# Optimization experiments

Measured on AMD Instinct MI355X. Metric: run time of the kernel, lower is better.

## Reference

```python
import jax, jax.numpy as jnp
import numpy as np

B, S, H, NH = 2, 2048, 2048, 16
DH = H // NH


def setup_inputs() -> dict:
    key = jax.random.key(0)
    ks = jax.random.split(key, 9)
    scale = 1.0 / np.sqrt(H)
    inp = {
        "hidden_state": jax.random.normal(ks[0], (B, S, H), dtype=jnp.float32),
        "Wq": jax.random.normal(ks[1], (H, H), dtype=jnp.float32) * scale,
        "bq": jnp.zeros((H,), dtype=jnp.float32),
        "Wk": jax.random.normal(ks[2], (H, H), dtype=jnp.float32) * scale,
        "bk": jnp.zeros((H,), dtype=jnp.float32),
        "Wv": jax.random.normal(ks[3], (H, H), dtype=jnp.float32) * scale,
        "bv": jnp.zeros((H,), dtype=jnp.float32),
        "Wo": jax.random.normal(ks[4], (H, H), dtype=jnp.float32) * scale,
        "bo": jnp.zeros((H,), dtype=jnp.float32),
    }
    # additive causal mask: 0 on/below diagonal, large negative above
    neg = jnp.float32(-1e9)
    tri = jnp.tril(jnp.ones((S, S), dtype=bool))
    inp["causal_mask"] = jnp.where(tri, 0.0, neg)[None, None, :, :]
    return inp


def reference(hidden_state, Wq, bq, Wk, bk, Wv, bv, Wo, bo, causal_mask):
    def split_heads(x):  # [B,S,H] -> [B,NH,S,DH]
        return x.reshape(B, S, NH, DH).transpose(0, 2, 1, 3)

    q = split_heads(hidden_state @ Wq + bq)
    k = split_heads(hidden_state @ Wk + bk)
    v = split_heads(hidden_state @ Wv + bv)

    scores = jnp.einsum("bhqd,bhkd->bhqk", q, k) / jnp.sqrt(jnp.float32(DH))
    scores = scores + causal_mask
    probs = jax.nn.softmax(scores, axis=-1)
    out = jnp.einsum("bhqk,bhkd->bhqd", probs, v)  # [B,NH,S,DH]
    out = out.transpose(0, 2, 1, 3).reshape(B, S, H)
    return out @ Wo + bo
```

## Files before the change

kernel.cpp:

```cpp
#include <hip/hip_runtime.h>
#include <cstdint>

typedef __attribute__((ext_vector_type(4))) float f32x4;
typedef __attribute__((ext_vector_type(16))) float f32x16;
typedef __attribute__((ext_vector_type(8))) __bf16 bf16x8;
typedef __attribute__((ext_vector_type(4))) unsigned short u16x4;
typedef __attribute__((ext_vector_type(2))) unsigned int u32x2;
typedef __attribute__((ext_vector_type(4))) float fvec4;

#define DEV __device__ __forceinline__
#define MFMA16(a, b, c) __builtin_amdgcn_mfma_f32_16x16x32_bf16((a), (b), (c), 0, 0, 0)
#define MFMA32(a, b, c) __builtin_amdgcn_mfma_f32_32x32x16_bf16((a), (b), (c), 0, 0, 0)

DEV unsigned short f2bf(float f) {
  union { float f; uint32_t u; } c; c.f = f;
  uint32_t u = c.u;
  return (unsigned short)((u + 0x7FFFu + ((u >> 16) & 1u)) >> 16);
}

DEV unsigned int pack2(float lo, float hi) {
  union { float f; uint32_t u; } a, b;
  a.f = lo; b.f = hi;
  return __builtin_amdgcn_perm(b.u + 0x8000u, a.u + 0x8000u, 0x07060302u);
}

DEV void gll16(const void* g, void* l) {
  __builtin_amdgcn_global_load_lds(
      (const __attribute__((address_space(1))) void*)(uintptr_t)g,
      (__attribute__((address_space(3))) void*)(uint32_t)(uintptr_t)l,
      16, 0, 0);
}

__global__ void cvt_bf16(const float* __restrict__ src, unsigned short* __restrict__ dst) {
  int i = (blockIdx.x * 256 + threadIdx.x) * 4;
  fvec4 v = *(const fvec4*)(src + i);
  u16x4 o;
  o[0] = f2bf(v[0]); o[1] = f2bf(v[1]); o[2] = f2bf(v[2]); o[3] = f2bf(v[3]);
  *(u16x4*)(dst + i) = o;
}

__global__ void transpose_cvt4(const float* __restrict__ W0, const float* __restrict__ W1,
                               const float* __restrict__ W2, const float* __restrict__ W3,
                               unsigned short* __restrict__ Dqkv, unsigned short* __restrict__ Do) {
  __shared__ float t[32][33];
  const float* W = blockIdx.z == 0 ? W0 : blockIdx.z == 1 ? W1 : blockIdx.z == 2 ? W2 : W3;
  unsigned short* WT = blockIdx.z < 3 ? Dqkv + (size_t)blockIdx.z * 2048 * 2048 : Do;
  int n0 = blockIdx.x * 32, k0 = blockIdx.y * 32;
  int x = threadIdx.x, y = threadIdx.y;
  #pragma unroll
  for (int i = 0; i < 32; i += 8)
    t[y + i][x] = W[(size_t)(k0 + y + i) * 2048 + n0 + x];
  __syncthreads();
  #pragma unroll
  for (int i = 0; i < 32; i += 8)
    WT[(size_t)(n0 + y + i) * 2048 + k0 + x] = f2bf(t[x][y + i]);
}

constexpr float QSC = 0.08838834764831845f * 1.4426950408889634f;

template <int MODE>
__global__ __launch_bounds__(256, 2) void gemm128(
    const unsigned short* __restrict__ A,
    const unsigned short* __restrict__ Bt,
    const float* __restrict__ b0, const float* __restrict__ b1,
    const float* __restrict__ b2,
    void* __restrict__ o0, void* __restrict__ o1, void* __restrict__ o2) {
  __shared__ unsigned short As[128 * 64];
  __shared__ unsigned short Bs[128 * 64];
  const int id = blockIdx.x;
  const int m0 = (((id & 7) << 2) | ((id >> 3) & 3)) * 128;
  const int n0 = (id >> 5) * 128;
  const int tid = threadIdx.x;
  const int wave = tid >> 6, lid = tid & 63;
  const int l16 = lid & 15, lq = lid >> 4;
  const int wm = (wave >> 1) * 64, wn = (wave & 1) * 64;

  const int srow = lid >> 3;
  const int sgrp = (lid & 7) ^ srow;

  f32x4 acc[4][4] = {};

  for (int k0 = 0; k0 < 2048; k0 += 64) {
    #pragma unroll
    for (int i = 0; i < 4; ++i) {
      const int t = wave * 4 + i;
      const int r = t * 8 + srow;
      gll16(A + (size_t)(m0 + r) * 2048 + k0 + sgrp * 8, (char*)As + t * 1024 + lid * 16);
      gll16(Bt + (size_t)(n0 + r) * 2048 + k0 + sgrp * 8, (char*)Bs + t * 1024 + lid * 16);
    }
    __syncthreads();
    #pragma unroll
    for (int kk = 0; kk < 2; ++kk) {
      const int G = kk * 4 + lq;
      bf16x8 af[4], bfr[4];
      #pragma unroll
      for (int i = 0; i < 4; ++i)
        af[i] = *(const bf16x8*)(As + (wm + i * 16 + l16) * 64 + ((G ^ (l16 & 7)) << 3));
      #pragma unroll
      for (int j = 0; j < 4; ++j)
        bfr[j] = *(const bf16x8*)(Bs + (wn + j * 16 + l16) * 64 + ((G ^ (l16 & 7)) << 3));
      #pragma unroll
      for (int i = 0; i < 4; ++i)
        #pragma unroll
        for (int j = 0; j < 4; ++j)
          acc[i][j] = MFMA16(af[i], bfr[j], acc[i][j]);
    }
    __syncthreads();
  }

  #pragma unroll
  for (int j = 0; j < 4; ++j) {
    const int c = n0 + wn + j * 16 + l16;
    if (MODE == 1) {
      const int which = c >> 11;
      const int hd = c & 2047;
      const int h = hd >> 7, d = hd & 127;
      const float* bp = which == 0 ? b0 : which == 1 ? b1 : b2;
      const float bv = bp[hd];
      if (which == 2) {
        #pragma unroll
        for (int i = 0; i < 4; ++i) {
          const int row0 = m0 + wm + i * 16 + lq * 4;
          const int bb = row0 >> 11, s0 = row0 & 2047;
          u16x4 pv;
          #pragma unroll
          for (int r = 0; r < 4; ++r) pv[r] = f2bf(acc[i][j][r] + bv);
          *(u16x4*)((unsigned short*)o2 + ((size_t)((bb * 16 + h) * 128 + d)) * 2048 + s0) = pv;
        }
      } else {
        const float sc = which == 0 ? QSC : 1.0f;
        unsigned short* op = which == 0 ? (unsigned short*)o0 : (unsigned short*)o1;
        #pragma unroll
        for (int i = 0; i < 4; ++i) {
          #pragma unroll
          for (int r = 0; r < 4; ++r) {
            const int row = m0 + wm + i * 16 + lq * 4 + r;
            const int bb = row >> 11, s = row & 2047;
            op[(size_t)((bb * 16 + h) * 2048 + s) * 128 + d] = f2bf((acc[i][j][r] + bv) * sc);
          }
        }
      }
    } else {
      const float bv = b0[c];
      #pragma unroll
      for (int i = 0; i < 4; ++i)
        #pragma unroll
        for (int r = 0; r < 4; ++r) {
          const int row = m0 + wm + i * 16 + lq * 4 + r;
          ((float*)o0)[(size_t)row * 2048 + c] = acc[i][j][r] + bv;
        }
    }
  }
}

__global__ __launch_bounds__(256, 2) void attn(
    const unsigned short* __restrict__ Q,
    const unsigned short* __restrict__ K,
    const unsigned short* __restrict__ Vt,
    unsigned short* __restrict__ ctx) {
  __shared__ unsigned short Ks[64 * 128];
  __shared__ unsigned short Vts[128 * 64];
  __shared__ unsigned short Ps[4 * 32 * 64];

  const int bh = blockIdx.y;
  const int jq = (bh < 16) ? (15 - (int)blockIdx.x) : (int)blockIdx.x;
  const int q0 = jq * 128;
  const int b = bh >> 4, h = bh & 15;
  const unsigned short* Qh = Q + (size_t)bh * 2048 * 128;
  const unsigned short* Kh = K + (size_t)bh * 2048 * 128;
  const unsigned short* Vth = Vt + (size_t)bh * 128 * 2048;

  const int tid = threadIdx.x;
  const int wave = tid >> 6, lid = tid & 63;
  const int l32 = lid & 31, half = lid >> 5;
  const int qrow = q0 + wave * 32 + l32;
  unsigned short* Pw = Ps + wave * 2048 + l32 * 64;
  const int qsw = l32 & 7;

  bf16x8 qf[8];
  #pragma unroll
  for (int ds = 0; ds < 8; ++ds)
    qf[ds] = *(const bf16x8*)(Qh + (size_t)qrow * 128 + ds * 16 + half * 8);

  float m_i = -1e30f, l_i = 0.f;
  f32x16 acc[4] = {};

  const int ntiles = 2 * jq + 2;
  for (int jt = 0; jt < ntiles; ++jt) {
    const int k0 = jt * 64;
    #pragma unroll
    for (int ii = 0; ii < 4; ++ii) {
      const int t = wave * 4 + ii;
      const int r = t * 4 + (lid >> 4);
      const int g = (lid & 15) ^ (r & 15);
      gll16(Kh + (size_t)(k0 + r) * 128 + g * 8, (char*)Ks + t * 1024 + lid * 16);
    }
    #pragma unroll
    for (int ii = 0; ii < 4; ++ii) {
      const int t = wave * 4 + ii;
      const int d = t * 8 + (lid >> 3);
      const int g = (lid & 7) ^ (d & 7);
      gll16(Vth + (size_t)d * 2048 + k0 + g * 8, (char*)Vts + t * 1024 + lid * 16);
    }
    __syncthreads();

    f32x16 sacc[2] = {};
    #pragma unroll
    for (int ds = 0; ds < 8; ++ds) {
      #pragma unroll
      for (int mb = 0; mb < 2; ++mb) {
        const int kr = mb * 32 + l32;
        bf16x8 af = *(const bf16x8*)(Ks + kr * 128 + (((ds * 2 + half) ^ (kr & 15)) << 3));
        sacc[mb] = MFMA32(af, qf[ds], sacc[mb]);
      }
    }

    if (jt >= 2 * jq) {
      #pragma unroll
      for (int mb = 0; mb < 2; ++mb)
        #pragma unroll
        for (int i = 0; i < 16; ++i) {
          const int kg = k0 + mb * 32 + (i & 3) + 8 * (i >> 2) + 4 * half;
          if (kg > qrow) sacc[mb][i] = -1e30f;
        }
    }

    float tmax = -1e30f;
    #pragma unroll
    for (int mb = 0; mb < 2; ++mb)
      #pragma unroll
      for (int i = 0; i < 16; ++i) tmax = fmaxf(tmax, sacc[mb][i]);
    tmax = fmaxf(tmax, __shfl_xor(tmax, 32));

    const float mnew = fmaxf(m_i, tmax);
    const float alpha = exp2f(m_i - mnew);
    m_i = mnew;

    float ps = 0.f;
    #pragma unroll
    for (int mb = 0; mb < 2; ++mb) {
      #pragma unroll
      for (int i = 0; i < 16; ++i) {
        sacc[mb][i] = exp2f(sacc[mb][i] - mnew);
        ps += sacc[mb][i];
      }
      #pragma unroll
      for (int u = 0; u < 4; ++u) {
        u32x2 w;
        w[0] = pack2(sacc[mb][4 * u], sacc[mb][4 * u + 1]);
        w[1] = pack2(sacc[mb][4 * u + 2], sacc[mb][4 * u + 3]);
        *(u32x2*)(Pw + (((u + mb * 4) ^ qsw) << 3) + half * 4) = w;
      }
    }
    ps += __shfl_xor(ps, 32);
    l_i = l_i * alpha + ps;
    #pragma unroll
    for (int db = 0; db < 4; ++db)
      #pragma unroll
      for (int i = 0; i < 16; ++i) acc[db][i] *= alpha;

    #pragma unroll
    for (int ks = 0; ks < 4; ++ks) {
      bf16x8 pf = *(const bf16x8*)(Pw + (((ks * 2 + half) ^ qsw) << 3));
      #pragma unroll
      for (int db = 0; db < 4; ++db) {
        const int d = db * 32 + l32;
        bf16x8 vf = *(const bf16x8*)(Vts + d * 64 + (((ks * 2 + half) ^ (d & 7)) << 3));
        acc[db] = MFMA32(vf, pf, acc[db]);
      }
    }
    __syncthreads();
  }

  const float inv = 1.f / l_i;
  const size_t base = ((size_t)(b * 2048 + qrow)) * 2048 + h * 128;
  #pragma unroll
  for (int db = 0; db < 4; ++db) {
    #pragma unroll
    for (int u = 0; u < 4; ++u) {
      u32x2 w;
      w[0] = pack2(acc[db][4 * u] * inv, acc[db][4 * u + 1] * inv);
      w[1] = pack2(acc[db][4 * u + 2] * inv, acc[db][4 * u + 3] * inv);
      *(u32x2*)(ctx + base + db * 32 + 8 * u + 4 * half) = w;
    }
  }
}

extern "C" void kernel_launch(void* const* d_in, const int* in_sizes, int n_in,
                              void* d_out, int out_size, void* d_ws, size_t ws_size,
                              hipStream_t stream) {
  const float* hs = (const float*)d_in[0];
  const float* Wq = (const float*)d_in[1];
  const float* bq = (const float*)d_in[2];
  const float* Wk = (const float*)d_in[3];
  const float* bk = (const float*)d_in[4];
  const float* Wv = (const float*)d_in[5];
  const float* bv = (const float*)d_in[6];
  const float* Wo = (const float*)d_in[7];
  const float* bo = (const float*)d_in[8];
  float* out = (float*)d_out;

  char* ws = (char*)d_ws;
  unsigned short* hsb   = (unsigned short*)(ws);
  unsigned short* wqkvt = (unsigned short*)(ws + (16 << 20));
  unsigned short* wot   = (unsigned short*)(ws + (40 << 20));
  unsigned short* Qb    = (unsigned short*)(ws + (48 << 20));
  unsigned short* Kb    = (unsigned short*)(ws + (64 << 20));
  unsigned short* Vtb   = (unsigned short*)(ws + (80 << 20));
  unsigned short* ctx   = (unsigned short*)(ws + (96 << 20));

  cvt_bf16<<<dim3(8192), dim3(256), 0, stream>>>(hs, hsb);
  transpose_cvt4<<<dim3(64, 64, 4), dim3(32, 8), 0, stream>>>(Wq, Wk, Wv, Wo, wqkvt, wot);

  gemm128<1><<<dim3(1536), 256, 0, stream>>>(hsb, wqkvt, bq, bk, bv,
                                             (void*)Qb, (void*)Kb, (void*)Vtb);
  attn<<<dim3(16, 32), 256, 0, stream>>>(Qb, Kb, Vtb, ctx);
  gemm128<0><<<dim3(512), 256, 0, stream>>>(ctx, wot, bo, nullptr, nullptr,
                                            (void*)out, nullptr, nullptr);
}
```

Baseline: 380.1 us.

## Halve attention query tile, pass P via lane shuffles, fuse prologue kernels

The attention kernel now uses 64-query blocks with 2 waves (128 threads) and a 32x32 grid, which doubles the block count for better load balance across the causal triangle. The new head-pair ordering also changes the work ordering. The probability tile no longer goes through LDS: P fragments are exchanged between wave halves with __shfl_xor, which removes the Ps buffer and its LDS traffic. The hidden-state conversion and the weight transposes are merged into one prologue launch. The cost is that each K/V tile is loaded by fewer waves per block, so each block issues more loads per tile and K/V reuse per block is lower.

```diff
diff --git a/kernel.cpp b/kernel.cpp
--- a/kernel.cpp
+++ b/kernel.cpp
@@ -31,17 +31,23 @@
       16, 0, 0);
 }
 
-__global__ void cvt_bf16(const float* __restrict__ src, unsigned short* __restrict__ dst) {
-  int i = (blockIdx.x * 256 + threadIdx.x) * 4;
-  fvec4 v = *(const fvec4*)(src + i);
-  u16x4 o;
-  o[0] = f2bf(v[0]); o[1] = f2bf(v[1]); o[2] = f2bf(v[2]); o[3] = f2bf(v[3]);
-  *(u16x4*)(dst + i) = o;
-}
-
-__global__ void transpose_cvt4(const float* __restrict__ W0, const float* __restrict__ W1,
-                               const float* __restrict__ W2, const float* __restrict__ W3,
-                               unsigned short* __restrict__ Dqkv, unsigned short* __restrict__ Do) {
+__global__ void prologue(const float* __restrict__ hs, unsigned short* __restrict__ hsb,
+                         const float* __restrict__ W0, const float* __restrict__ W1,
+                         const float* __restrict__ W2, const float* __restrict__ W3,
+                         unsigned short* __restrict__ Dqkv, unsigned short* __restrict__ Do) {
+  const int tid = threadIdx.y * 32 + threadIdx.x;
+  if (blockIdx.z == 4) {
+    const int id = blockIdx.y * 64 + blockIdx.x;
+    int i = (id * 256 + tid) * 8;
+    #pragma unroll
+    for (int u = 0; u < 2; ++u) {
+      fvec4 v = *(const fvec4*)(hs + i + u * 4);
+      u16x4 o;
+      o[0] = f2bf(v[0]); o[1] = f2bf(v[1]); o[2] = f2bf(v[2]); o[3] = f2bf(v[3]);
+      *(u16x4*)(hsb + i + u * 4) = o;
+    }
+    return;
+  }
   __shared__ float t[32][33];
   const float* W = blockIdx.z == 0 ? W0 : blockIdx.z == 1 ? W1 : blockIdx.z == 2 ? W2 : W3;
   unsigned short* WT = blockIdx.z < 3 ? Dqkv + (size_t)blockIdx.z * 2048 * 2048 : Do;
@@ -153,18 +159,17 @@
   }
 }
 
-__global__ __launch_bounds__(256, 2) void attn(
+__global__ __launch_bounds__(128, 2) void attn(
     const unsigned short* __restrict__ Q,
     const unsigned short* __restrict__ K,
     const unsigned short* __restrict__ Vt,
     unsigned short* __restrict__ ctx) {
   __shared__ unsigned short Ks[64 * 128];
   __shared__ unsigned short Vts[128 * 64];
-  __shared__ unsigned short Ps[4 * 32 * 64];
 
   const int bh = blockIdx.y;
-  const int jq = (bh < 16) ? (15 - (int)blockIdx.x) : (int)blockIdx.x;
-  const int q0 = jq * 128;
+  const int jq = (bh & 8) ? (int)blockIdx.x : 31 - (int)blockIdx.x;
+  const int q0 = jq * 64;
   const int b = bh >> 4, h = bh & 15;
   const unsigned short* Qh = Q + (size_t)bh * 2048 * 128;
   const unsigned short* Kh = K + (size_t)bh * 2048 * 128;
@@ -174,8 +179,6 @@
   const int wave = tid >> 6, lid = tid & 63;
   const int l32 = lid & 31, half = lid >> 5;
   const int qrow = q0 + wave * 32 + l32;
-  unsigned short* Pw = Ps + wave * 2048 + l32 * 64;
-  const int qsw = l32 & 7;
 
   bf16x8 qf[8];
   #pragma unroll
@@ -185,19 +188,18 @@
   float m_i = -1e30f, l_i = 0.f;
   f32x16 acc[4] = {};
 
-  const int ntiles = 2 * jq + 2;
-  for (int jt = 0; jt < ntiles; ++jt) {
+  for (int jt = 0; jt <= jq; ++jt) {
     const int k0 = jt * 64;
     #pragma unroll
-    for (int ii = 0; ii < 4; ++ii) {
-      const int t = wave * 4 + ii;
+    for (int ii = 0; ii < 8; ++ii) {
+      const int t = wave * 8 + ii;
       const int r = t * 4 + (lid >> 4);
       const int g = (lid & 15) ^ (r & 15);
       gll16(Kh + (size_t)(k0 + r) * 128 + g * 8, (char*)Ks + t * 1024 + lid * 16);
     }
     #pragma unroll
-    for (int ii = 0; ii < 4; ++ii) {
-      const int t = wave * 4 + ii;
+    for (int ii = 0; ii < 8; ++ii) {
+      const int t = wave * 8 + ii;
       const int d = t * 8 + (lid >> 3);
       const int g = (lid & 7) ^ (d & 7);
       gll16(Vth + (size_t)d * 2048 + k0 + g * 8, (char*)Vts + t * 1024 + lid * 16);
@@ -215,7 +217,7 @@
       }
     }
 
-    if (jt >= 2 * jq) {
+    if (jt == jq) {
       #pragma unroll
       for (int mb = 0; mb < 2; ++mb)
         #pragma unroll
@@ -235,8 +237,13 @@
     const float mnew = fmaxf(m_i, tmax);
     const float alpha = exp2f(m_i - mnew);
     m_i = mnew;
+    #pragma unroll
+    for (int db = 0; db < 4; ++db)
+      #pragma unroll
+      for (int i = 0; i < 16; ++i) acc[db][i] *= alpha;
 
     float ps = 0.f;
+    u32x2 pk[2][4];
     #pragma unroll
     for (int mb = 0; mb < 2; ++mb) {
       #pragma unroll
@@ -246,27 +253,34 @@
       }
       #pragma unroll
       for (int u = 0; u < 4; ++u) {
-        u32x2 w;
-        w[0] = pack2(sacc[mb][4 * u], sacc[mb][4 * u + 1]);
-        w[1] = pack2(sacc[mb][4 * u + 2], sacc[mb][4 * u + 3]);
-        *(u32x2*)(Pw + (((u + mb * 4) ^ qsw) << 3) + half * 4) = w;
+        pk[mb][u][0] = pack2(sacc[mb][4 * u], sacc[mb][4 * u + 1]);
+        pk[mb][u][1] = pack2(sacc[mb][4 * u + 2], sacc[mb][4 * u + 3]);
       }
     }
     ps += __shfl_xor(ps, 32);
     l_i = l_i * alpha + ps;
-    #pragma unroll
-    for (int db = 0; db < 4; ++db)
-      #pragma unroll
-      for (int i = 0; i < 16; ++i) acc[db][i] *= alpha;
-
-    #pragma unroll
-    for (int ks = 0; ks < 4; ++ks) {
-      bf16x8 pf = *(const bf16x8*)(Pw + (((ks * 2 + half) ^ qsw) << 3));
+
+    #pragma unroll
+    for (int g = 0; g < 4; ++g) {
+      const int mb = g >> 1, u0 = (g & 1) * 2;
+      u32x2 vx, own;
+      vx[0] = half ? pk[mb][u0][0] : pk[mb][u0 + 1][0];
+      vx[1] = half ? pk[mb][u0][1] : pk[mb][u0 + 1][1];
+      own[0] = half ? pk[mb][u0 + 1][0] : pk[mb][u0][0];
+      own[1] = half ? pk[mb][u0 + 1][1] : pk[mb][u0][1];
+      u32x2 r;
+      r[0] = __shfl_xor((unsigned int)vx[0], 32);
+      r[1] = __shfl_xor((unsigned int)vx[1], 32);
+      union { unsigned int u[4]; bf16x8 v; } pf;
+      pf.u[0] = half ? r[0] : own[0];
+      pf.u[1] = half ? r[1] : own[1];
+      pf.u[2] = half ? own[0] : r[0];
+      pf.u[3] = half ? own[1] : r[1];
       #pragma unroll
       for (int db = 0; db < 4; ++db) {
         const int d = db * 32 + l32;
-        bf16x8 vf = *(const bf16x8*)(Vts + d * 64 + (((ks * 2 + half) ^ (d & 7)) << 3));
-        acc[db] = MFMA32(vf, pf, acc[db]);
+        bf16x8 vf = *(const bf16x8*)(Vts + d * 64 + (((g * 2 + half) ^ (d & 7)) << 3));
+        acc[db] = MFMA32(vf, pf.v, acc[db]);
       }
     }
     __syncthreads();
@@ -309,12 +323,11 @@
   unsigned short* Vtb   = (unsigned short*)(ws + (80 << 20));
   unsigned short* ctx   = (unsigned short*)(ws + (96 << 20));
 
-  cvt_bf16<<<dim3(8192), dim3(256), 0, stream>>>(hs, hsb);
-  transpose_cvt4<<<dim3(64, 64, 4), dim3(32, 8), 0, stream>>>(Wq, Wk, Wv, Wo, wqkvt, wot);
+  prologue<<<dim3(64, 64, 5), dim3(32, 8), 0, stream>>>(hs, hsb, Wq, Wk, Wv, Wo, wqkvt, wot);
 
   gemm128<1><<<dim3(1536), 256, 0, stream>>>(hsb, wqkvt, bq, bk, bv,
                                              (void*)Qb, (void*)Kb, (void*)Vtb);
-  attn<<<dim3(16, 32), 256, 0, stream>>>(Qb, Kb, Vtb, ctx);
+  attn<<<dim3(32, 32), 128, 0, stream>>>(Qb, Kb, Vtb, ctx);
   gemm128<0><<<dim3(512), 256, 0, stream>>>(ctx, wot, bo, nullptr, nullptr,
                                             (void*)out, nullptr, nullptr);
 }
```

Result: slower. 417.1 us (+9.8%).
